# Optimization experiments

Measured on AMD Instinct MI355X. Metric: run time of the kernel, lower is better.

The kernel has to match this reference:

```python
import jax, jax.numpy as jnp
import numpy as np

B = 64
H_FS = W_FS = 56
IN_DIM, OUT_DIM, NUM_HEADS = 96, 192, 2
HEAD_DIM = OUT_DIM // NUM_HEADS  # 96
STRIDE_Q, STRIDE_KV = (2, 2), (4, 4)
REL_RANGE = 2 * (H_FS // STRIDE_Q[0]) - 1  # 55
LN_EPS = 1e-5


def setup_inputs() -> dict:
    key = jax.random.key(0)
    ks = jax.random.split(key, 12)
    N = H_FS * W_FS + 1  # +1 cls token
    s = 0.02
    d = {
        "hidden_states": jax.random.normal(ks[0], (B, N, IN_DIM), jnp.float32),
        "Wq": jax.random.normal(ks[1], (IN_DIM, OUT_DIM), jnp.float32) * s,
        "bq": jnp.zeros((OUT_DIM,), jnp.float32),
        "Wk": jax.random.normal(ks[2], (IN_DIM, OUT_DIM), jnp.float32) * s,
        "bk": jnp.zeros((OUT_DIM,), jnp.float32),
        "Wv": jax.random.normal(ks[3], (IN_DIM, OUT_DIM), jnp.float32) * s,
        "bv": jnp.zeros((OUT_DIM,), jnp.float32),
        # depthwise pool convs: (C_out=C, C_in/groups=1, kh, kw)
        "pool_q_w": jax.random.normal(ks[4], (IN_DIM, 1, 3, 3), jnp.float32) * 0.1,
        "pool_k_w": jax.random.normal(ks[5], (IN_DIM, 1, 3, 3), jnp.float32) * 0.1,
        "pool_v_w": jax.random.normal(ks[6], (IN_DIM, 1, 3, 3), jnp.float32) * 0.1,
        "gq": jnp.ones((IN_DIM,), jnp.float32), "betaq": jnp.zeros((IN_DIM,), jnp.float32),
        "gk": jnp.ones((IN_DIM,), jnp.float32), "betak": jnp.zeros((IN_DIM,), jnp.float32),
        "gv": jnp.ones((IN_DIM,), jnp.float32), "betav": jnp.zeros((IN_DIM,), jnp.float32),
        "rel_h": jax.random.normal(ks[7], (REL_RANGE, HEAD_DIM), jnp.float32) * s,
        "rel_w": jax.random.normal(ks[8], (REL_RANGE, HEAD_DIM), jnp.float32) * s,
        "height": H_FS,
        "width": W_FS,
    }
    return d


def _layernorm(x, g, b):
    m = x.mean(-1, keepdims=True)
    v = ((x - m) ** 2).mean(-1, keepdims=True)
    return (x - m) * jax.lax.rsqrt(v + LN_EPS) * g + b


def _pool(x, w, stride, g, b, height, width):
    # x: (B, folds=1, N, C) with cls token first
    bsz, _, _, C = x.shape
    cls_tok, rest = x[:, :, :1], x[:, :, 1:]
    sp = rest.reshape(bsz, height, width, C).transpose(0, 3, 1, 2)  # (B, C, H, W)
    y = jax.lax.conv_general_dilated(
        sp, w, stride, [(1, 1), (1, 1)], feature_group_count=C,
        dimension_numbers=("NCHW", "OIHW", "NCHW"))
    hp, wp = y.shape[2], y.shape[3]
    y = y.reshape(bsz, 1, C, hp * wp).transpose(0, 1, 3, 2)  # (B, 1, N', C)
    y = jnp.concatenate([cls_tok, y], axis=2)
    return _layernorm(y, g, b), (hp, wp)


def _rel_idx(qn, kn):
    q_ratio = max(kn / qn, 1.0)
    k_ratio = max(qn / kn, 1.0)
    dist = (np.arange(qn)[:, None] * q_ratio - np.arange(kn)[None, :] * k_ratio
            + (kn - 1) * k_ratio)
    return dist.astype(np.int64)


def reference(hidden_states, Wq, bq, Wk, bk, Wv, bv, pool_q_w, pool_k_w, pool_v_w,
              gq, betaq, gk, betak, gv, betav, rel_h, rel_w, height, width):
    bsz, N, C = hidden_states.shape
    h = hidden_states.reshape(bsz, N, 1, C).transpose(0, 2, 1, 3)  # (B, folds=1, N, C)

    q, (qh, qw) = _pool(h, pool_q_w, STRIDE_Q, gq, betaq, height, width)
    k, (kh, kw) = _pool(h, pool_k_w, STRIDE_KV, gk, betak, height, width)
    v, _ = _pool(h, pool_v_w, STRIDE_KV, gv, betav, height, width)

    def proj(x, W, bias, n):
        x = x.transpose(0, 2, 1, 3).reshape(bsz, n, -1)
        x = x @ W + bias
        return x.reshape(bsz, n, NUM_HEADS, HEAD_DIM).transpose(0, 2, 1, 3)

    nq, nk = qh * qw + 1, kh * kw + 1
    q = proj(q, Wq, bq, nq)  # (B, H, nq, d)
    k = proj(k, Wk, bk, nk)
    v = proj(v, Wv, bv, nk)

    scale = HEAD_DIM ** -0.5
    attn = jnp.einsum("bhqd,bhkd->bhqk", q * scale, k)

    # decomposed spatial relative positional bias (cls offset = 1)
    Rh = rel_h[_rel_idx(qh, kh)]  # (qh, kh, d)
    Rw = rel_w[_rel_idx(qw, kw)]  # (qw, kw, d)
    rq = q[:, :, 1:].reshape(bsz, NUM_HEADS, qh, qw, HEAD_DIM)
    eh = jnp.einsum("byhwc,hkc->byhwk", rq, Rh)
    ew = jnp.einsum("byhwc,wkc->byhwk", rq, Rw)
    blk = (attn[:, :, 1:, 1:].reshape(bsz, NUM_HEADS, qh, qw, kh, kw)
           + eh[..., :, None] + ew[..., None, :])
    attn = attn.at[:, :, 1:, 1:].set(blk.reshape(bsz, NUM_HEADS, qh * qw, kh * kw))

    attn = jax.nn.softmax(attn, axis=-1)
    out = jnp.einsum("bhqk,bhkd->bhqd", attn, v)
    out = out.at[:, :, 1:].add(q[:, :, 1:])  # residual pooling (skip cls)
    return out.transpose(0, 2, 1, 3).reshape(bsz, nq, OUT_DIM)
```

## Files before the change

### kernel.cpp

```cpp
#include <hip/hip_runtime.h>
#include <hip/hip_bf16.h>

#define B_    64
#define HFS   56
#define CIN   96
#define NQ    785
#define NK    197
#define QW    28
#define KW    14
#define NTOT  3137
#define NQP   800
#define NKP   208
#define NKPV  224
#define VROWS 112
#define KSCL  0.10206207261596575f

typedef __attribute__((ext_vector_type(8))) short short8;
typedef __attribute__((ext_vector_type(4))) short shortx4;
typedef __attribute__((ext_vector_type(4))) float floatx4;

__device__ __forceinline__ short f2s(float x) {
    __hip_bfloat16 h = __float2bfloat16(x);
    return *reinterpret_cast<short*>(&h);
}
__device__ __forceinline__ float s2f(short s) {
    __hip_bfloat16 h; *reinterpret_cast<short*>(&h) = s;
    return __bfloat162float(h);
}
__device__ __forceinline__ short8 ld8(const short* p) {
    return *reinterpret_cast<const short8*>(p);
}

#define MFMA16(a,b,c) __builtin_amdgcn_mfma_f32_16x16x32_bf16((a),(b),(c),0,0,0)

__global__ void prep_kernel(const float* __restrict__ Wq, const float* __restrict__ Wk,
                            const float* __restrict__ Wv, const float* __restrict__ relh,
                            const float* __restrict__ relw,
                            const float* __restrict__ pqw, const float* __restrict__ pkw,
                            const float* __restrict__ pvw,
                            short* __restrict__ WTq, short* __restrict__ WTk,
                            short* __restrict__ WTv, short* __restrict__ relc,
                            short* __restrict__ vt,
                            float* __restrict__ cwqT, float* __restrict__ cwkT,
                            float* __restrict__ cwvT)
{
    int i = blockIdx.x * 256 + threadIdx.x;
    if (i < 18432)      { int o = i/96, c = i%96;              WTq[o*96+c] = f2s(Wq[c*192+o]); }
    else if (i < 36864) { int j = i-18432; int o=j/96,c=j%96;  WTk[o*96+c] = f2s(Wk[c*192+o]*KSCL); }
    else if (i < 55296) { int j = i-36864; int o=j/96,c=j%96;  WTv[o*96+c] = f2s(Wv[c*192+o]); }
    else if (i < 66048) {
        int j = i - 55296;  int r = j/96, c = j%96;
        float v = (r < 54) ? relh[r*96+c] : ((r < 108) ? relw[(r-54)*96+c] : 0.f);
        relc[r*96+c] = f2s(v);
    } else if (i < 721408) {
        int j2 = i - 66048;
        int bh = j2 / 5120, r = j2 % 5120;
        int row, tok; short val;
        if (r < 3584) { row = 96 + r/224; tok = r%224;
                        val = (row == 96 && tok < NK) ? (short)0x3F80 : (short)0; }
        else          { int rr = r-3584; row = rr/16; tok = 208 + (rr%16); val = 0; }
        vt[((long)bh*VROWS + row)*NKPV + tok] = val;
    } else if (i < 724000) {
        int j = i - 721408;
        int w = j / 864, r = j % 864;
        int c = r / 9, off = r % 9;
        const float* src = (w == 0) ? pqw : (w == 1) ? pkw : pvw;
        float*       dst = (w == 0) ? cwqT : (w == 1) ? cwkT : cwvT;
        dst[off*96 + c] = src[c*9 + off];
    }
}

__device__ __forceinline__ void ln_store2(float xa, float xb, bool act,
    const float* __restrict__ g, const float* __restrict__ beta,
    short* __restrict__ outp, int c)
{
    float s  = act ? (xa + xb) : 0.f;
    float ss = act ? (xa*xa + xb*xb) : 0.f;
    #pragma unroll
    for (int off = 32; off >= 1; off >>= 1) {
        s  += __shfl_xor(s,  off, 64);
        ss += __shfl_xor(ss, off, 64);
    }
    float m   = s / CIN;
    float var = ss / CIN - m*m;
    float r   = rsqrtf(var + 1e-5f);
    if (act) {
        float2 g2 = *reinterpret_cast<const float2*>(g + c);
        float2 b2 = *reinterpret_cast<const float2*>(beta + c);
        unsigned pa = (unsigned short)f2s((xa - m)*r*g2.x + b2.x);
        unsigned pb = (unsigned short)f2s((xb - m)*r*g2.y + b2.y);
        *reinterpret_cast<unsigned*>(outp + c) = pa | (pb << 16);
    }
}

__global__ __launch_bounds__(256) void pool_ln_kernel(
    const float* __restrict__ hs,
    const float* __restrict__ cwqT, const float* __restrict__ cwkT, const float* __restrict__ cwvT,
    const float* __restrict__ gq, const float* __restrict__ betaq,
    const float* __restrict__ gk, const float* __restrict__ betak,
    const float* __restrict__ gv, const float* __restrict__ betav,
    short* __restrict__ pq, short* __restrict__ pk, short* __restrict__ pv)
{
    int wid  = threadIdx.x >> 6;
    int lane = threadIdx.x & 63;
    int gid  = blockIdx.x * 4 + wid;
    int b = gid / 1008;
    int t = gid % 1008;
    bool act = (lane < 48);
    int c = lane * 2;
    const long hb = (long)b * NTOT * CIN;

    if (t < NQP) {
        short* outp = pq + ((long)b*NQP + t)*CIN;
        if (t >= NQ) { if (act) *reinterpret_cast<unsigned*>(outp + c) = 0u; return; }
        float xa = 0.f, xb = 0.f;
        if (t == 0) {
            if (act) { float2 h2 = *reinterpret_cast<const float2*>(hs + hb + c); xa = h2.x; xb = h2.y; }
        } else {
            int j = t - 1, oy = j / QW, ox = j % QW;
            #pragma unroll
            for (int dy = 0; dy < 3; ++dy) {
                int iy = oy*2 - 1 + dy;
                if (iy < 0 || iy >= HFS) continue;
                #pragma unroll
                for (int dx = 0; dx < 3; ++dx) {
                    int ix = ox*2 - 1 + dx;
                    if (ix < 0 || ix >= HFS) continue;
                    if (act) {
                        long base = hb + (long)(1 + iy*HFS + ix) * CIN;
                        float2 h2 = *reinterpret_cast<const float2*>(hs + base + c);
                        float2 w2 = *reinterpret_cast<const float2*>(cwqT + (dy*3+dx)*96 + c);
                        xa = fmaf(h2.x, w2.x, xa);
                        xb = fmaf(h2.y, w2.y, xb);
                    }
                }
            }
        }
        ln_store2(xa, xb, act, gq, betaq, outp, c);
    } else {
        int tok = t - NQP;
        short* ok_ = pk + ((long)b*NKP + tok)*CIN;
        short* ov_ = pv + ((long)b*NKP + tok)*CIN;
        if (tok >= NK) {
            if (act) {
                *reinterpret_cast<unsigned*>(ok_ + c) = 0u;
                *reinterpret_cast<unsigned*>(ov_ + c) = 0u;
            }
            return;
        }
        float ka = 0.f, kb_ = 0.f, va = 0.f, vb = 0.f;
        if (tok == 0) {
            if (act) {
                float2 h2 = *reinterpret_cast<const float2*>(hs + hb + c);
                ka = va = h2.x;  kb_ = vb = h2.y;
            }
        } else {
            int j = tok - 1, oy = j / KW, ox = j % KW;
            #pragma unroll
            for (int dy = 0; dy < 3; ++dy) {
                int iy = oy*4 - 1 + dy;
                if (iy < 0 || iy >= HFS) continue;
                #pragma unroll
                for (int dx = 0; dx < 3; ++dx) {
                    int ix = ox*4 - 1 + dx;
                    if (ix < 0 || ix >= HFS) continue;
                    if (act) {
                        long base = hb + (long)(1 + iy*HFS + ix) * CIN;
                        int wo = (dy*3+dx)*96 + c;
                        float2 h2 = *reinterpret_cast<const float2*>(hs + base + c);
                        float2 wk2 = *reinterpret_cast<const float2*>(cwkT + wo);
                        float2 wv2 = *reinterpret_cast<const float2*>(cwvT + wo);
                        ka  = fmaf(h2.x, wk2.x, ka);
                        kb_ = fmaf(h2.y, wk2.y, kb_);
                        va  = fmaf(h2.x, wv2.x, va);
                        vb  = fmaf(h2.y, wv2.y, vb);
                    }
                }
            }
        }
        ln_store2(ka, kb_, act, gk, betak, ok_, c);
        ln_store2(va, vb, act, gv, betav, ov_, c);
    }
}

__global__ __launch_bounds__(256) void proj_mfma_kernel(
    const short* __restrict__ pq, const short* __restrict__ pk, const short* __restrict__ pv,
    const short* __restrict__ WTq, const short* __restrict__ WTk, const short* __restrict__ WTv,
    const float* __restrict__ bq, const float* __restrict__ bk, const float* __restrict__ bv,
    short* __restrict__ qb, short* __restrict__ kb, short* __restrict__ vt)
{
    int wid  = threadIdx.x >> 6;
    int lane = threadIdx.x & 63;
    int quad = lane >> 4, col = lane & 15;
    int wt = blockIdx.x * 4 + wid;

    if (wt < 4032) {
        const short *A, *WT; const float* bias; short* outp;
        int ntokp, row0; float bsc;
        if (wt < 3200) { A = pq; WT = WTq; bias = bq; outp = qb; ntokp = NQP; row0 = wt*16; bsc = 1.f; }
        else           { A = pk; WT = WTk; bias = bk; outp = kb; ntokp = NKP; row0 = (wt-3200)*16; bsc = KSCL; }

        short8 bt[3];
        #pragma unroll
        for (int cc = 0; cc < 3; ++cc)
            bt[cc] = ld8(A + (long)(row0 + col)*96 + cc*32 + quad*8);

        int b = row0 / ntokp;
        int tok = (row0 % ntokp) + col;

        #pragma unroll
        for (int nt = 0; nt < 12; ++nt) {
            floatx4 acc = {0.f, 0.f, 0.f, 0.f};
            #pragma unroll
            for (int cc = 0; cc < 3; ++cc) {
                short8 af = ld8(WT + (nt*16 + col)*96 + cc*32 + quad*8);
                acc = MFMA16(af, bt[cc], acc);
            }
            int o0 = nt*16 + quad*4;
            float4 bo = *reinterpret_cast<const float4*>(bias + o0);
            int h  = (o0 >= 96) ? 1 : 0;
            int d0 = o0 - h*96;
            shortx4 val;
            val.x = f2s(acc[0] + bo.x*bsc);
            val.y = f2s(acc[1] + bo.y*bsc);
            val.z = f2s(acc[2] + bo.z*bsc);
            val.w = f2s(acc[3] + bo.w*bsc);
            *reinterpret_cast<shortx4*>(outp + ((long)(b*2 + h)*ntokp + tok)*96 + d0) = val;
        }
    } else {
        int row0 = (wt - 4032) * 16;
        short8 at[3];
        #pragma unroll
        for (int cc = 0; cc < 3; ++cc)
            at[cc] = ld8(pv + (long)(row0 + col)*96 + cc*32 + quad*8);

        int b = row0 / NKP;
        int tloc0 = (row0 % NKP) + quad*4;

        #pragma unroll
        for (int nt = 0; nt < 12; ++nt) {
            floatx4 acc = {0.f, 0.f, 0.f, 0.f};
            #pragma unroll
            for (int cc = 0; cc < 3; ++cc) {
                short8 bf = ld8(WTv + (nt*16 + col)*96 + cc*32 + quad*8);
                acc = MFMA16(at[cc], bf, acc);
            }
            int o = nt*16 + col;
            int h = (o >= 96) ? 1 : 0;
            int d = o - h*96;
            float bo = bv[o];
            shortx4 val;
            val.x = (tloc0+0 < NK) ? f2s(acc[0] + bo) : (short)0;
            val.y = (tloc0+1 < NK) ? f2s(acc[1] + bo) : (short)0;
            val.z = (tloc0+2 < NK) ? f2s(acc[2] + bo) : (short)0;
            val.w = (tloc0+3 < NK) ? f2s(acc[3] + bo) : (short)0;
            *reinterpret_cast<shortx4*>(vt + ((long)(b*2 + h)*VROWS + d)*NKPV + tloc0) = val;
        }
    }
}

__global__ __launch_bounds__(256) void attn_kernel(
    const short* __restrict__ qb, const short* __restrict__ kb,
    const short* __restrict__ vt, const short* __restrict__ relc,
    float* __restrict__ out)
{
    __shared__ short e_s[4][16][112];
    __shared__ __align__(16) short p_s[4][16][232];

    int tid  = threadIdx.x;
    int wid  = tid >> 6;
    int lane = tid & 63;
    int quad = lane >> 4, col = lane & 15;

    int bid = blockIdx.x;
    int tb  = (bid & 7) * 200 + (bid >> 3);
    int wt  = tb * 4 + wid;
    int bh  = wt / 50;
    int t   = wt % 50;
    int q0  = t * 16;

    const short* qrow = qb + ((long)bh*NQP + q0)*96;
    short8 aq[3];
    #pragma unroll
    for (int c = 0; c < 3; ++c)
        aq[c] = ld8(qrow + col*96 + c*32 + quad*8);

    #pragma unroll
    for (int rt = 0; rt < 7; ++rt) {
        floatx4 acc = {0.f, 0.f, 0.f, 0.f};
        #pragma unroll
        for (int c = 0; c < 3; ++c) {
            short8 bf = ld8(relc + (rt*16 + col)*96 + c*32 + quad*8);
            acc = MFMA16(aq[c], bf, acc);
        }
        #pragma unroll
        for (int reg = 0; reg < 4; ++reg)
            e_s[wid][quad*4 + reg][rt*16 + col] = f2s(acc[reg]);
    }

    int qyo[4], qxo[4];
    #pragma unroll
    for (int reg = 0; reg < 4; ++reg) {
        int qq = q0 + quad*4 + reg;
        int jj = (qq > 0) ? (qq - 1) : 0;
        qyo[reg] = jj / QW;
        qxo[reg] = jj % QW;
    }

    const short* kbase = kb + (long)bh*NKP*96;
    #pragma unroll
    for (int kt = 0; kt < 13; ++kt) {
        floatx4 acc = {0.f, 0.f, 0.f, 0.f};
        #pragma unroll
        for (int c = 0; c < 3; ++c) {
            short8 bf = ld8(kbase + (kt*16 + col)*96 + c*32 + quad*8);
            acc = MFMA16(aq[c], bf, acc);
        }
        int k  = kt*16 + col;
        int kk = (k > 0) ? (k - 1) : 0;
        int ky = kk / 14;  ky = (ky < 13) ? ky : 13;
        int kx = kk - 14*ky;
        int oh = 26 - 2*ky;
        int ow2 = 26 - 2*kx;
        #pragma unroll
        for (int reg = 0; reg < 4; ++reg) {
            const short* er = &e_s[wid][quad*4 + reg][0];
            float bias = s2f(er[qyo[reg] + oh]) + s2f(er[54 + qxo[reg] + ow2]);
            if (kt == 0) bias = (col == 0) ? 0.f : bias;
            if (q0 == 0 && reg == 0) bias = (quad == 0) ? 0.f : bias;
            p_s[wid][quad*4 + reg][k] = f2s(__expf(acc[reg] + bias));
        }
    }
    #pragma unroll
    for (int reg = 0; reg < 4; ++reg)
        p_s[wid][quad*4 + reg][208 + col] = 0;

    floatx4 o[7];
    #pragma unroll
    for (int nt = 0; nt < 7; ++nt) o[nt] = floatx4{0.f, 0.f, 0.f, 0.f};
    const short* vbase = vt + (long)bh*VROWS*NKPV;
    #pragma unroll
    for (int c = 0; c < 7; ++c) {
        short8 ap = ld8(&p_s[wid][col][c*32 + quad*8]);
        #pragma unroll
        for (int nt = 0; nt < 7; ++nt) {
            short8 bf = ld8(vbase + (nt*16 + col)*NKPV + c*32 + quad*8);
            o[nt] = MFMA16(ap, bf, o[nt]);
        }
    }

    float inv[4];
    #pragma unroll
    for (int reg = 0; reg < 4; ++reg) {
        float srow = __shfl(o[6][reg], lane & 48, 64);
        inv[reg] = 1.0f / srow;
    }
    int b = bh >> 1, h = bh & 1;
    #pragma unroll
    for (int nt = 0; nt < 6; ++nt) {
        int ch = nt*16 + col;
        #pragma unroll
        for (int reg = 0; reg < 4; ++reg) {
            int q = q0 + quad*4 + reg;
            if (q < NQ) {
                float val = o[nt][reg] * inv[reg];
                if (q > 0) val += s2f(qb[((long)bh*NQP + q)*96 + ch]);
                out[((long)b*NQ + q)*192 + h*96 + ch] = val;
            }
        }
    }
}

extern "C" void kernel_launch(void* const* d_in, const int* in_sizes, int n_in,
                              void* d_out, int out_size, void* d_ws, size_t ws_size,
                              hipStream_t stream)
{
    const float* hs    = (const float*)d_in[0];
    const float* Wq    = (const float*)d_in[1];
    const float* bq    = (const float*)d_in[2];
    const float* Wk    = (const float*)d_in[3];
    const float* bk    = (const float*)d_in[4];
    const float* Wv    = (const float*)d_in[5];
    const float* bv    = (const float*)d_in[6];
    const float* pqw   = (const float*)d_in[7];
    const float* pkw   = (const float*)d_in[8];
    const float* pvw   = (const float*)d_in[9];
    const float* gq    = (const float*)d_in[10];
    const float* betaq = (const float*)d_in[11];
    const float* gk    = (const float*)d_in[12];
    const float* betak = (const float*)d_in[13];
    const float* gv    = (const float*)d_in[14];
    const float* betav = (const float*)d_in[15];
    const float* relh  = (const float*)d_in[16];
    const float* relw  = (const float*)d_in[17];
    float* out = (float*)d_out;

    short* pq   = (short*)d_ws;
    short* pk   = pq  + (long)B_*NQP*CIN;
    short* pv   = pk  + (long)B_*NKP*CIN;
    short* qb   = pv  + (long)B_*NKP*CIN;
    short* kb   = qb  + (long)128*NQP*96;
    short* vt   = kb  + (long)128*NKP*96;
    short* WTq  = vt  + (long)128*VROWS*NKPV;
    short* WTk  = WTq + 192*96;
    short* WTv  = WTk + 192*96;
    short* relc = WTv + 192*96;
    float* cwqT = (float*)(relc + 112*96);
    float* cwkT = cwqT + 9*96;
    float* cwvT = cwkT + 9*96;

    prep_kernel<<<2829, 256, 0, stream>>>(Wq, Wk, Wv, relh, relw,
                                          pqw, pkw, pvw,
                                          WTq, WTk, WTv, relc, vt,
                                          cwqT, cwkT, cwvT);

    pool_ln_kernel<<<(B_*1008)/4, 256, 0, stream>>>(
        hs, cwqT, cwkT, cwvT, gq, betaq, gk, betak, gv, betav, pq, pk, pv);

    proj_mfma_kernel<<<4864/4, 256, 0, stream>>>(
        pq, pk, pv, WTq, WTk, WTv, bq, bk, bv, qb, kb, vt);

    attn_kernel<<<1600, 256, 0, stream>>>(qb, kb, vt, relc, out);
}
```

Before: 278.9 us.

## Pack four tokens per wave in pool_ln and alias attention bias/prob LDS buffers

The pool+layernorm kernel now assigns 16 lanes per token, each handling 6 channels, so a wave processes four tokens instead of one token with 16 idle lanes. The LN reduction shrinks to a 16-lane shuffle, and the grid is reduced by 4x. In the attention kernel, the relative-position bias for all 13 key tiles is precomputed into fp16-packed registers first, which lets the bias buffer and the probability buffer share one LDS array and cuts shared memory per block. The trade-offs are more registers and fp16 rounding of the bias terms.

Measured after the change: 258.3 us. -7.4%, faster.

```diff
diff --git a/kernel.cpp b/kernel.cpp
--- a/kernel.cpp
+++ b/kernel.cpp
@@ -1,5 +1,6 @@
 #include <hip/hip_runtime.h>
 #include <hip/hip_bf16.h>
+#include <hip/hip_fp16.h>
 
 #define B_    64
 #define HFS   56
@@ -29,6 +30,21 @@
 }
 __device__ __forceinline__ short8 ld8(const short* p) {
     return *reinterpret_cast<const short8*>(p);
+}
+__device__ __forceinline__ unsigned pkbf(float a, float b) {
+    return (unsigned)(unsigned short)f2s(a) | ((unsigned)(unsigned short)f2s(b) << 16);
+}
+__device__ __forceinline__ unsigned pkhf(float a, float b) {
+    __half2 h = __floats2half2_rn(a, b);
+    return *reinterpret_cast<unsigned*>(&h);
+}
+__device__ __forceinline__ float hflo(unsigned w) {
+    __half2 h = *reinterpret_cast<__half2*>(&w);
+    return __half2float(__low2half(h));
+}
+__device__ __forceinline__ float hfhi(unsigned w) {
+    __half2 h = *reinterpret_cast<__half2*>(&w);
+    return __half2float(__high2half(h));
 }
 
 #define MFMA16(a,b,c) __builtin_amdgcn_mfma_f32_16x16x32_bf16((a),(b),(c),0,0,0)
@@ -70,27 +86,36 @@
     }
 }
 
-__device__ __forceinline__ void ln_store2(float xa, float xb, bool act,
+__device__ __forceinline__ void red16_2(float& s, float& ss) {
+    #pragma unroll
+    for (int off = 8; off >= 1; off >>= 1) {
+        s  += __shfl_xor(s,  off, 16);
+        ss += __shfl_xor(ss, off, 16);
+    }
+}
+
+__device__ __forceinline__ void ln6_store(const float* x, float m, float r,
     const float* __restrict__ g, const float* __restrict__ beta,
-    short* __restrict__ outp, int c)
-{
-    float s  = act ? (xa + xb) : 0.f;
-    float ss = act ? (xa*xa + xb*xb) : 0.f;
-    #pragma unroll
-    for (int off = 32; off >= 1; off >>= 1) {
-        s  += __shfl_xor(s,  off, 64);
-        ss += __shfl_xor(ss, off, 64);
-    }
-    float m   = s / CIN;
-    float var = ss / CIN - m*m;
-    float r   = rsqrtf(var + 1e-5f);
-    if (act) {
-        float2 g2 = *reinterpret_cast<const float2*>(g + c);
-        float2 b2 = *reinterpret_cast<const float2*>(beta + c);
-        unsigned pa = (unsigned short)f2s((xa - m)*r*g2.x + b2.x);
-        unsigned pb = (unsigned short)f2s((xb - m)*r*g2.y + b2.y);
-        *reinterpret_cast<unsigned*>(outp + c) = pa | (pb << 16);
-    }
+    int c0, short* __restrict__ outp)
+{
+    float2 g0 = *reinterpret_cast<const float2*>(g + c0);
+    float2 g1 = *reinterpret_cast<const float2*>(g + c0 + 2);
+    float2 g2 = *reinterpret_cast<const float2*>(g + c0 + 4);
+    float2 b0 = *reinterpret_cast<const float2*>(beta + c0);
+    float2 b1 = *reinterpret_cast<const float2*>(beta + c0 + 2);
+    float2 b2 = *reinterpret_cast<const float2*>(beta + c0 + 4);
+    unsigned o0 = pkbf((x[0]-m)*r*g0.x + b0.x, (x[1]-m)*r*g0.y + b0.y);
+    unsigned o1 = pkbf((x[2]-m)*r*g1.x + b1.x, (x[3]-m)*r*g1.y + b1.y);
+    unsigned o2 = pkbf((x[4]-m)*r*g2.x + b2.x, (x[5]-m)*r*g2.y + b2.y);
+    *reinterpret_cast<unsigned*>(outp)     = o0;
+    *reinterpret_cast<unsigned*>(outp + 2) = o1;
+    *reinterpret_cast<unsigned*>(outp + 4) = o2;
+}
+
+__device__ __forceinline__ void zero6(short* __restrict__ outp) {
+    *reinterpret_cast<unsigned*>(outp)     = 0u;
+    *reinterpret_cast<unsigned*>(outp + 2) = 0u;
+    *reinterpret_cast<unsigned*>(outp + 4) = 0u;
 }
 
 __global__ __launch_bounds__(256) void pool_ln_kernel(
@@ -101,85 +126,120 @@
     const float* __restrict__ gv, const float* __restrict__ betav,
     short* __restrict__ pq, short* __restrict__ pk, short* __restrict__ pv)
 {
-    int wid  = threadIdx.x >> 6;
-    int lane = threadIdx.x & 63;
-    int gid  = blockIdx.x * 4 + wid;
-    int b = gid / 1008;
-    int t = gid % 1008;
-    bool act = (lane < 48);
-    int c = lane * 2;
-    const long hb = (long)b * NTOT * CIN;
-
-    if (t < NQP) {
-        short* outp = pq + ((long)b*NQP + t)*CIN;
-        if (t >= NQ) { if (act) *reinterpret_cast<unsigned*>(outp + c) = 0u; return; }
-        float xa = 0.f, xb = 0.f;
+    const int wid  = threadIdx.x >> 6;
+    const int lane = threadIdx.x & 63;
+    const int sub  = lane >> 4;
+    const int li   = lane & 15;
+    const int c0   = li * 6;
+    const int gid  = blockIdx.x * 4 + wid;
+    const int b    = gid / 252;
+    const int slot = gid % 252;
+    const long hb  = (long)b * NTOT * CIN;
+
+    if (slot < 200) {
+        int t = slot*4 + sub;
+        short* outp = pq + ((long)b*NQP + t)*CIN + c0;
+        if (t >= NQ) { zero6(outp); return; }
+        float x[6];
+        #pragma unroll
+        for (int i = 0; i < 6; ++i) x[i] = 0.f;
         if (t == 0) {
-            if (act) { float2 h2 = *reinterpret_cast<const float2*>(hs + hb + c); xa = h2.x; xb = h2.y; }
+            const float* hp = hs + hb + c0;
+            float2 a0 = *reinterpret_cast<const float2*>(hp);
+            float2 a1 = *reinterpret_cast<const float2*>(hp + 2);
+            float2 a2 = *reinterpret_cast<const float2*>(hp + 4);
+            x[0]=a0.x; x[1]=a0.y; x[2]=a1.x; x[3]=a1.y; x[4]=a2.x; x[5]=a2.y;
         } else {
             int j = t - 1, oy = j / QW, ox = j % QW;
             #pragma unroll
             for (int dy = 0; dy < 3; ++dy) {
                 int iy = oy*2 - 1 + dy;
-                if (iy < 0 || iy >= HFS) continue;
                 #pragma unroll
                 for (int dx = 0; dx < 3; ++dx) {
                     int ix = ox*2 - 1 + dx;
-                    if (ix < 0 || ix >= HFS) continue;
-                    if (act) {
-                        long base = hb + (long)(1 + iy*HFS + ix) * CIN;
-                        float2 h2 = *reinterpret_cast<const float2*>(hs + base + c);
-                        float2 w2 = *reinterpret_cast<const float2*>(cwqT + (dy*3+dx)*96 + c);
-                        xa = fmaf(h2.x, w2.x, xa);
-                        xb = fmaf(h2.y, w2.y, xb);
+                    if (iy >= 0 && iy < HFS && ix >= 0 && ix < HFS) {
+                        const float* hp = hs + hb + (long)(1 + iy*HFS + ix)*CIN + c0;
+                        const float* wp = cwqT + (dy*3+dx)*96 + c0;
+                        float2 h0 = *reinterpret_cast<const float2*>(hp);
+                        float2 h1 = *reinterpret_cast<const float2*>(hp + 2);
+                        float2 h2 = *reinterpret_cast<const float2*>(hp + 4);
+                        float2 w0 = *reinterpret_cast<const float2*>(wp);
+                        float2 w1 = *reinterpret_cast<const float2*>(wp + 2);
+                        float2 w2 = *reinterpret_cast<const float2*>(wp + 4);
+                        x[0] = fmaf(h0.x, w0.x, x[0]); x[1] = fmaf(h0.y, w0.y, x[1]);
+                        x[2] = fmaf(h1.x, w1.x, x[2]); x[3] = fmaf(h1.y, w1.y, x[3]);
+                        x[4] = fmaf(h2.x, w2.x, x[4]); x[5] = fmaf(h2.y, w2.y, x[5]);
                     }
                 }
             }
         }
-        ln_store2(xa, xb, act, gq, betaq, outp, c);
+        float s  = (x[0]+x[1]) + (x[2]+x[3]) + (x[4]+x[5]);
+        float ss = fmaf(x[0],x[0], fmaf(x[1],x[1], fmaf(x[2],x[2],
+                   fmaf(x[3],x[3], fmaf(x[4],x[4], x[5]*x[5])))));
+        red16_2(s, ss);
+        float m   = s * (1.f/96.f);
+        float var = ss * (1.f/96.f) - m*m;
+        float r   = rsqrtf(var + 1e-5f);
+        ln6_store(x, m, r, gq, betaq, c0, outp);
     } else {
-        int tok = t - NQP;
-        short* ok_ = pk + ((long)b*NKP + tok)*CIN;
-        short* ov_ = pv + ((long)b*NKP + tok)*CIN;
-        if (tok >= NK) {
-            if (act) {
-                *reinterpret_cast<unsigned*>(ok_ + c) = 0u;
-                *reinterpret_cast<unsigned*>(ov_ + c) = 0u;
-            }
-            return;
-        }
-        float ka = 0.f, kb_ = 0.f, va = 0.f, vb = 0.f;
+        int tok = (slot - 200)*4 + sub;
+        short* ok_ = pk + ((long)b*NKP + tok)*CIN + c0;
+        short* ov_ = pv + ((long)b*NKP + tok)*CIN + c0;
+        if (tok >= NK) { zero6(ok_); zero6(ov_); return; }
+        float xk[6], xv[6];
+        #pragma unroll
+        for (int i = 0; i < 6; ++i) { xk[i] = 0.f; xv[i] = 0.f; }
         if (tok == 0) {
-            if (act) {
-                float2 h2 = *reinterpret_cast<const float2*>(hs + hb + c);
-                ka = va = h2.x;  kb_ = vb = h2.y;
-            }
+            const float* hp = hs + hb + c0;
+            float2 a0 = *reinterpret_cast<const float2*>(hp);
+            float2 a1 = *reinterpret_cast<const float2*>(hp + 2);
+            float2 a2 = *reinterpret_cast<const float2*>(hp + 4);
+            xk[0]=xv[0]=a0.x; xk[1]=xv[1]=a0.y; xk[2]=xv[2]=a1.x;
+            xk[3]=xv[3]=a1.y; xk[4]=xv[4]=a2.x; xk[5]=xv[5]=a2.y;
         } else {
             int j = tok - 1, oy = j / KW, ox = j % KW;
             #pragma unroll
             for (int dy = 0; dy < 3; ++dy) {
                 int iy = oy*4 - 1 + dy;
-                if (iy < 0 || iy >= HFS) continue;
                 #pragma unroll
                 for (int dx = 0; dx < 3; ++dx) {
                     int ix = ox*4 - 1 + dx;
-                    if (ix < 0 || ix >= HFS) continue;
-                    if (act) {
-                        long base = hb + (long)(1 + iy*HFS + ix) * CIN;
-                        int wo = (dy*3+dx)*96 + c;
-                        float2 h2 = *reinterpret_cast<const float2*>(hs + base + c);
-                        float2 wk2 = *reinterpret_cast<const float2*>(cwkT + wo);
-                        float2 wv2 = *reinterpret_cast<const float2*>(cwvT + wo);
-                        ka  = fmaf(h2.x, wk2.x, ka);
-                        kb_ = fmaf(h2.y, wk2.y, kb_);
-                        va  = fmaf(h2.x, wv2.x, va);
-                        vb  = fmaf(h2.y, wv2.y, vb);
+                    if (iy >= 0 && iy < HFS && ix >= 0 && ix < HFS) {
+                        const float* hp = hs + hb + (long)(1 + iy*HFS + ix)*CIN + c0;
+                        int wo = (dy*3+dx)*96 + c0;
+                        float2 h0 = *reinterpret_cast<const float2*>(hp);
+                        float2 h1 = *reinterpret_cast<const float2*>(hp + 2);
+                        float2 h2 = *reinterpret_cast<const float2*>(hp + 4);
+                        float2 k0 = *reinterpret_cast<const float2*>(cwkT + wo);
+                        float2 k1 = *reinterpret_cast<const float2*>(cwkT + wo + 2);
+                        float2 k2 = *reinterpret_cast<const float2*>(cwkT + wo + 4);
+                        float2 v0 = *reinterpret_cast<const float2*>(cwvT + wo);
+                        float2 v1 = *reinterpret_cast<const float2*>(cwvT + wo + 2);
+                        float2 v2 = *reinterpret_cast<const float2*>(cwvT + wo + 4);
+                        xk[0] = fmaf(h0.x, k0.x, xk[0]); xk[1] = fmaf(h0.y, k0.y, xk[1]);
+                        xk[2] = fmaf(h1.x, k1.x, xk[2]); xk[3] = fmaf(h1.y, k1.y, xk[3]);
+                        xk[4] = fmaf(h2.x, k2.x, xk[4]); xk[5] = fmaf(h2.y, k2.y, xk[5]);
+                        xv[0] = fmaf(h0.x, v0.x, xv[0]); xv[1] = fmaf(h0.y, v0.y, xv[1]);
+                        xv[2] = fmaf(h1.x, v1.x, xv[2]); xv[3] = fmaf(h1.y, v1.y, xv[3]);
+                        xv[4] = fmaf(h2.x, v2.x, xv[4]); xv[5] = fmaf(h2.y, v2.y, xv[5]);
                     }
                 }
             }
         }
-        ln_store2(ka, kb_, act, gk, betak, ok_, c);
-        ln_store2(va, vb, act, gv, betav, ov_, c);
+        float sk  = (xk[0]+xk[1]) + (xk[2]+xk[3]) + (xk[4]+xk[5]);
+        float ssk = fmaf(xk[0],xk[0], fmaf(xk[1],xk[1], fmaf(xk[2],xk[2],
+                    fmaf(xk[3],xk[3], fmaf(xk[4],xk[4], xk[5]*xk[5])))));
+        float sv  = (xv[0]+xv[1]) + (xv[2]+xv[3]) + (xv[4]+xv[5]);
+        float ssv = fmaf(xv[0],xv[0], fmaf(xv[1],xv[1], fmaf(xv[2],xv[2],
+                    fmaf(xv[3],xv[3], fmaf(xv[4],xv[4], xv[5]*xv[5])))));
+        red16_2(sk, ssk);
+        red16_2(sv, ssv);
+        float mk = sk * (1.f/96.f), vark = ssk * (1.f/96.f) - mk*mk;
+        float mv = sv * (1.f/96.f), varv = ssv * (1.f/96.f) - mv*mv;
+        float rk = rsqrtf(vark + 1e-5f);
+        float rv = rsqrtf(varv + 1e-5f);
+        ln6_store(xk, mk, rk, gk, betak, c0, ok_);
+        ln6_store(xv, mv, rv, gv, betav, c0, ov_);
     }
 }
 
@@ -264,8 +324,7 @@
     const short* __restrict__ vt, const short* __restrict__ relc,
     float* __restrict__ out)
 {
-    __shared__ short e_s[4][16][112];
-    __shared__ __align__(16) short p_s[4][16][232];
+    __shared__ __align__(16) short smem[4][16][232];
 
     int tid  = threadIdx.x;
     int wid  = tid >> 6;
@@ -295,7 +354,7 @@
         }
         #pragma unroll
         for (int reg = 0; reg < 4; ++reg)
-            e_s[wid][quad*4 + reg][rt*16 + col] = f2s(acc[reg]);
+            smem[wid][quad*4 + reg][rt*16 + col] = f2s(acc[reg]);
     }
 
     int qyo[4], qxo[4];
@@ -307,33 +366,47 @@
         qxo[reg] = jj % QW;
     }
 
-    const short* kbase = kb + (long)bh*NKP*96;
+    unsigned bpk[13][2];
     #pragma unroll
     for (int kt = 0; kt < 13; ++kt) {
-        floatx4 acc = {0.f, 0.f, 0.f, 0.f};
-        #pragma unroll
-        for (int c = 0; c < 3; ++c) {
-            short8 bf = ld8(kbase + (kt*16 + col)*96 + c*32 + quad*8);
-            acc = MFMA16(aq[c], bf, acc);
-        }
         int k  = kt*16 + col;
         int kk = (k > 0) ? (k - 1) : 0;
         int ky = kk / 14;  ky = (ky < 13) ? ky : 13;
         int kx = kk - 14*ky;
-        int oh = 26 - 2*ky;
+        int oh  = 26 - 2*ky;
         int ow2 = 26 - 2*kx;
+        float bs[4];
         #pragma unroll
         for (int reg = 0; reg < 4; ++reg) {
-            const short* er = &e_s[wid][quad*4 + reg][0];
+            const short* er = &smem[wid][quad*4 + reg][0];
             float bias = s2f(er[qyo[reg] + oh]) + s2f(er[54 + qxo[reg] + ow2]);
             if (kt == 0) bias = (col == 0) ? 0.f : bias;
             if (q0 == 0 && reg == 0) bias = (quad == 0) ? 0.f : bias;
-            p_s[wid][quad*4 + reg][k] = f2s(__expf(acc[reg] + bias));
-        }
+            bs[reg] = bias;
+        }
+        bpk[kt][0] = pkhf(bs[0], bs[1]);
+        bpk[kt][1] = pkhf(bs[2], bs[3]);
+    }
+
+    const short* kbase = kb + (long)bh*NKP*96;
+    #pragma unroll
+    for (int kt = 0; kt < 13; ++kt) {
+        floatx4 acc = {0.f, 0.f, 0.f, 0.f};
+        #pragma unroll
+        for (int c = 0; c < 3; ++c) {
+            short8 bf = ld8(kbase + (kt*16 + col)*96 + c*32 + quad*8);
+            acc = MFMA16(aq[c], bf, acc);
+        }
+        int k = kt*16 + col;
+        unsigned w0 = bpk[kt][0], w1 = bpk[kt][1];
+        smem[wid][quad*4 + 0][k] = f2s(__expf(acc[0] + hflo(w0)));
+        smem[wid][quad*4 + 1][k] = f2s(__expf(acc[1] + hfhi(w0)));
+        smem[wid][quad*4 + 2][k] = f2s(__expf(acc[2] + hflo(w1)));
+        smem[wid][quad*4 + 3][k] = f2s(__expf(acc[3] + hfhi(w1)));
     }
     #pragma unroll
     for (int reg = 0; reg < 4; ++reg)
-        p_s[wid][quad*4 + reg][208 + col] = 0;
+        smem[wid][quad*4 + reg][208 + col] = 0;
 
     floatx4 o[7];
     #pragma unroll
@@ -341,7 +414,7 @@
     const short* vbase = vt + (long)bh*VROWS*NKPV;
     #pragma unroll
     for (int c = 0; c < 7; ++c) {
-        short8 ap = ld8(&p_s[wid][col][c*32 + quad*8]);
+        short8 ap = ld8(&smem[wid][col][c*32 + quad*8]);
         #pragma unroll
         for (int nt = 0; nt < 7; ++nt) {
             short8 bf = ld8(vbase + (nt*16 + col)*NKPV + c*32 + quad*8);
@@ -414,7 +487,7 @@
                                           WTq, WTk, WTv, relc, vt,
                                           cwqT, cwkT, cwvT);
 
-    pool_ln_kernel<<<(B_*1008)/4, 256, 0, stream>>>(
+    pool_ln_kernel<<<(B_*1008)/16, 256, 0, stream>>>(
         hs, cwqT, cwkT, cwvT, gq, betaq, gk, betak, gv, betav, pq, pk, pv);
 
     proj_mfma_kernel<<<4864/4, 256, 0, stream>>>(
```
